# Kernel tuning notes

Hardware: AMD Instinct MI355X
Metric: run time of the kernel (lower is better)

## Reference

```python
import jax, jax.numpy as jnp
import numpy as np

SIGMA = 0.1
RHO = 10.0
B = 8
F = 64


def quad_linear(x, sigma=SIGMA):
    lin = 2.0 * x / sigma + 1.0
    quad = (x / sigma) ** 2 + 2.0 * x / sigma + 1.0
    return jnp.where(x > 0, lin, jnp.where(x >= -sigma, quad, jnp.zeros_like(x)))


def heaviside(x):
    return (x > 0).astype(x.dtype)


def setup_inputs() -> dict:
    key = jax.random.key(0)
    k1, k2, k3, k4 = jax.random.split(key, 4)
    sim_matrix = jax.random.normal(k1, (B, B, F, F), dtype=jnp.float32)
    pseudo_pos = jax.random.randint(k2, (B, B, F, F), 0, 2).astype(jnp.float32)
    pseudo_neg = jax.random.randint(k3, (B, B, F, F), 0, 2).astype(jnp.float32)
    label = jax.random.randint(k4, (B, B), 0, 2).astype(jnp.float32)
    return {
        "sim_matrix": sim_matrix,
        "pseudo_pos_label_matrix": pseudo_pos,
        "pseudo_neg_label_matrix": pseudo_neg,
        "label_matrix": label,
    }


def reference(sim_matrix, pseudo_pos_label_matrix, pseudo_neg_label_matrix, label_matrix):
    sigma, rho = SIGMA, RHO
    # off-diagonal mask over the last two (j,k) frame axes: [F,F]
    mask = 1.0 - jnp.eye(F, dtype=sim_matrix.dtype)
    # sim_diff[b1,b2,i,j,k] = sim[b1,b2,i,k] - sim[b1,b2,i,j]  -> [B,B,F,F,F]
    sim_diff = sim_matrix[..., None, :] - sim_matrix[..., :, None]
    pos = pseudo_pos_label_matrix
    neg = pseudo_neg_label_matrix
    # pos_pos[b1,b2,i,j,k] = pos[...,i,k]*pos[...,i,j]
    pos_pos = pos[..., None, :] * pos[..., :, None]
    # pos_neg[b1,b2,i,j,k] = neg[...,i,k]*pos[...,i,j]
    pos_neg = neg[..., None, :] * pos[..., :, None]
    sim_sl = jnp.where(pos_neg == 1.0, quad_linear(sim_diff, sigma), jnp.zeros_like(sim_diff))
    sim_sl = sim_sl * mask
    sim_sl_sg = jnp.where(pos_pos == 1.0, rho * heaviside(sim_diff), sim_sl)
    sim_sl_sg = sim_sl_sg * mask
    sim_all_rk = jnp.sum(sim_sl_sg, axis=-1) + 1.0                 # [B,B,F,F]
    sim_pos_sg = jnp.where(pos_pos == 1.0, sim_sl_sg, jnp.zeros_like(sim_sl_sg))
    sim_pos_rk = jnp.sum(sim_pos_sg, axis=-1) + 1.0                # [B,B,F,F]
    pos_divide_vec = jnp.sum(sim_pos_rk / sim_all_rk * pos, axis=-1)  # [B,B,F]
    pos_cnt_vec = jnp.sum(pos, axis=-1)                               # [B,B,F]
    ap_matrix = jnp.mean(pos_divide_vec / pos_cnt_vec, axis=-1)       # [B,B]
    pos_ap_matrix = ap_matrix * label_matrix
    ap = jnp.sum(pos_ap_matrix) / jnp.sum(label_matrix)
    return 1.0 - ap
```

## Files before the change

### kernel.cpp

```cpp
#include <hip/hip_runtime.h>

#define SIGMA 0.1f
#define RHO   10.0f
#define B     8
#define F     64

__global__ __launch_bounds__(64) void row_kernel(
    const float* __restrict__ sim,
    const float* __restrict__ pos,
    const float* __restrict__ neg,
    float* __restrict__ r_out)
{
    const int row = blockIdx.x;
    const int j   = threadIdx.x;

    __shared__ float ls[F];
    __shared__ float lp[F];
    __shared__ float ln[F];

    const size_t base = (size_t)row * F;
    ls[j] = sim[base + j];
    lp[j] = pos[base + j];
    ln[j] = neg[base + j];
    __syncthreads();

    const float sj  = ls[j];
    const bool  pj1 = lp[j] > 0.5f;

    float all_acc = 0.0f;
    float pos_acc = 0.0f;

    #pragma unroll 8
    for (int k = 0; k < F; ++k) {
        const float d   = ls[k] - sj;
        const bool  pk  = lp[k] > 0.5f;
        const bool  nk  = ln[k] > 0.5f;
        const bool  pp  = pj1 && pk;
        const bool  pn  = pj1 && nk;

        float val;
        if (pp) {
            val = (d > 0.0f) ? RHO : 0.0f;
        } else if (pn) {
            const float xs = d * (1.0f / SIGMA);
            if (d > 0.0f)            val = 2.0f * xs + 1.0f;
            else if (d >= -SIGMA)    val = xs * xs + 2.0f * xs + 1.0f;
            else                     val = 0.0f;
        } else {
            val = 0.0f;
        }
        if (k == j) val = 0.0f;

        all_acc += val;
        pos_acc += pp ? val : 0.0f;
    }

    const float all_rk = all_acc + 1.0f;
    const float pos_rk = pos_acc + 1.0f;

    float term = (pos_rk / all_rk) * (pj1 ? 1.0f : 0.0f);
    float cnt  = pj1 ? 1.0f : 0.0f;

    #pragma unroll
    for (int off = 32; off > 0; off >>= 1) {
        term += __shfl_down(term, off, 64);
        cnt  += __shfl_down(cnt,  off, 64);
    }

    if (j == 0) r_out[row] = term / cnt;
}

__global__ __launch_bounds__(64) void finish_kernel(
    const float* __restrict__ r,
    const float* __restrict__ label,
    float* __restrict__ out)
{
    const int p = threadIdx.x;

    float acc = 0.0f;
    #pragma unroll 8
    for (int i = 0; i < F; ++i) acc += r[p * F + i];
    const float ap  = acc * (1.0f / F);
    const float lab = label[p];

    float s1 = ap * lab;
    float s2 = lab;
    #pragma unroll
    for (int off = 32; off > 0; off >>= 1) {
        s1 += __shfl_down(s1, off, 64);
        s2 += __shfl_down(s2, off, 64);
    }

    if (p == 0) out[0] = 1.0f - s1 / s2;
}

extern "C" void kernel_launch(void* const* d_in, const int* in_sizes, int n_in,
                              void* d_out, int out_size, void* d_ws, size_t ws_size,
                              hipStream_t stream)
{
    const float* sim   = (const float*)d_in[0];
    const float* pos   = (const float*)d_in[1];
    const float* neg   = (const float*)d_in[2];
    const float* label = (const float*)d_in[3];
    float*       out   = (float*)d_out;
    float*       r     = (float*)d_ws;

    row_kernel<<<B * B * F, 64, 0, stream>>>(sim, pos, neg, r);
    finish_kernel<<<1, 64, 0, stream>>>(r, label, out);
}
```

Baseline: 72.65 us.

## Use wave ballots to skip non-contributing columns and pack four rows per block

```diff
diff --git a/kernel.cpp b/kernel.cpp
--- a/kernel.cpp
+++ b/kernel.cpp
@@ -4,94 +4,100 @@
 #define RHO   10.0f
 #define B     8
 #define F     64
+#define ROWS_PER_BLOCK 4
 
-__global__ __launch_bounds__(64) void row_kernel(
+__global__ __launch_bounds__(256) void row_kernel(
     const float* __restrict__ sim,
     const float* __restrict__ pos,
     const float* __restrict__ neg,
-    float* __restrict__ r_out)
+    const float* __restrict__ label,
+    float* __restrict__ partial)
 {
-    const int row = blockIdx.x;
-    const int j   = threadIdx.x;
+    const int lane = threadIdx.x & 63;
+    const int w    = threadIdx.x >> 6;
+    const int row  = blockIdx.x * ROWS_PER_BLOCK + w;
+    const int pair = row >> 6;
 
-    __shared__ float ls[F];
-    __shared__ float lp[F];
-    __shared__ float ln[F];
+    __shared__ float ls[ROWS_PER_BLOCK][F];
+    __shared__ float psum[ROWS_PER_BLOCK];
 
     const size_t base = (size_t)row * F;
-    ls[j] = sim[base + j];
-    lp[j] = pos[base + j];
-    ln[j] = neg[base + j];
-    __syncthreads();
+    const float sj = sim[base + lane];
+    const float pj = pos[base + lane];
+    const float nj = neg[base + lane];
+    ls[w][lane] = sj;
 
-    const float sj  = ls[j];
-    const bool  pj1 = lp[j] > 0.5f;
+    const unsigned long long pmask = __ballot(pj > 0.5f);
+    const unsigned long long nonly = __ballot(nj > 0.5f) & ~pmask;
 
     float all_acc = 0.0f;
     float pos_acc = 0.0f;
 
-    #pragma unroll 8
     for (int k = 0; k < F; ++k) {
-        const float d   = ls[k] - sj;
-        const bool  pk  = lp[k] > 0.5f;
-        const bool  nk  = ln[k] > 0.5f;
-        const bool  pp  = pj1 && pk;
-        const bool  pn  = pj1 && nk;
-
-        float val;
-        if (pp) {
-            val = (d > 0.0f) ? RHO : 0.0f;
-        } else if (pn) {
+        if ((pmask >> k) & 1ull) {
+            const float d = ls[w][k] - sj;
+            const float v = (d > 0.0f) ? RHO : 0.0f;
+            all_acc += v;
+            pos_acc += v;
+        } else if ((nonly >> k) & 1ull) {
+            const float d  = ls[w][k] - sj;
             const float xs = d * (1.0f / SIGMA);
-            if (d > 0.0f)            val = 2.0f * xs + 1.0f;
-            else if (d >= -SIGMA)    val = xs * xs + 2.0f * xs + 1.0f;
-            else                     val = 0.0f;
-        } else {
-            val = 0.0f;
+            const float t  = xs + 1.0f;
+            const float v  = (d > 0.0f) ? fmaf(2.0f, xs, 1.0f)
+                                        : ((t >= 0.0f) ? t * t : 0.0f);
+            all_acc += v;
         }
-        if (k == j) val = 0.0f;
-
-        all_acc += val;
-        pos_acc += pp ? val : 0.0f;
     }
 
     const float all_rk = all_acc + 1.0f;
     const float pos_rk = pos_acc + 1.0f;
 
-    float term = (pos_rk / all_rk) * (pj1 ? 1.0f : 0.0f);
-    float cnt  = pj1 ? 1.0f : 0.0f;
+    float term = (pj > 0.5f) ? (pos_rk / all_rk) : 0.0f;
+    float cntv = (pj > 0.5f) ? 1.0f : 0.0f;
 
     #pragma unroll
     for (int off = 32; off > 0; off >>= 1) {
         term += __shfl_down(term, off, 64);
-        cnt  += __shfl_down(cnt,  off, 64);
+        cntv += __shfl_down(cntv, off, 64);
     }
 
-    if (j == 0) r_out[row] = term / cnt;
+    if (lane == 0) psum[w] = term / cntv;
+    __syncthreads();
+
+    if (threadIdx.x == 0) {
+        const float lab = label[pair];
+        const float s = psum[0] + psum[1] + psum[2] + psum[3];
+        partial[blockIdx.x] = s * (1.0f / F) * lab;
+    }
 }
 
-__global__ __launch_bounds__(64) void finish_kernel(
-    const float* __restrict__ r,
+__global__ __launch_bounds__(256) void finish_kernel(
+    const float* __restrict__ partial,
     const float* __restrict__ label,
     float* __restrict__ out)
 {
-    const int p = threadIdx.x;
+    const int t    = threadIdx.x;
+    const int lane = t & 63;
+    const int w    = t >> 6;
 
-    float acc = 0.0f;
-    #pragma unroll 8
-    for (int i = 0; i < F; ++i) acc += r[p * F + i];
-    const float ap  = acc * (1.0f / F);
-    const float lab = label[p];
+    const float4 v = ((const float4*)partial)[t];
+    float s = v.x + v.y + v.z + v.w;
+    #pragma unroll
+    for (int off = 32; off > 0; off >>= 1) s += __shfl_down(s, off, 64);
 
-    float s1 = ap * lab;
-    float s2 = lab;
-    #pragma unroll
-    for (int off = 32; off > 0; off >>= 1) {
-        s1 += __shfl_down(s1, off, 64);
-        s2 += __shfl_down(s2, off, 64);
+    __shared__ float sm[4];
+    if (lane == 0) sm[w] = s;
+    __syncthreads();
+
+    if (t < 64) {
+        float den = label[t];
+        #pragma unroll
+        for (int off = 32; off > 0; off >>= 1) den += __shfl_down(den, off, 64);
+        if (t == 0) {
+            const float num = sm[0] + sm[1] + sm[2] + sm[3];
+            out[0] = 1.0f - num / den;
+        }
     }
-
-    if (p == 0) out[0] = 1.0f - s1 / s2;
 }
 
 extern "C" void kernel_launch(void* const* d_in, const int* in_sizes, int n_in,
@@ -103,8 +109,8 @@
     const float* neg   = (const float*)d_in[2];
     const float* label = (const float*)d_in[3];
     float*       out   = (float*)d_out;
-    float*       r     = (float*)d_ws;
+    float*       part  = (float*)d_ws;
 
-    row_kernel<<<B * B * F, 64, 0, stream>>>(sim, pos, neg, r);
-    finish_kernel<<<1, 64, 0, stream>>>(r, label, out);
+    row_kernel<<<(B * B * F) / ROWS_PER_BLOCK, 256, 0, stream>>>(sim, pos, neg, label, part);
+    finish_kernel<<<1, 256, 0, stream>>>(part, label, out);
 }
```

Result: faster. 68.34 us, median of 2 (-5.9%).
